# Optimization experiments

Hardware: AMD Instinct MI355X
Metric: run time of the kernel (lower is better)

The kernel has to match this reference:

```python
import jax, jax.numpy as jnp
import numpy as np

H = 128; F = 64; G = 50; L = 4; CUT = 10.0
M = 256; K = 8; A = 32
N_TOPO = M * A; N = M * K * A; NCONF = M * K
E_CONF = N * 16; E_GRAPH = N_TOPO * 4
ATOM_TYPES = 100; BOND_TYPES = 10
OFFSETS = jnp.linspace(0.0, CUT, G)
GCOEFF = -0.5 / (CUT / (G - 1)) ** 2  # GaussianSmearing coeff
BN_EPS = 1e-5


def batchnorm(x, g, b):
    # BatchNorm1d in training mode: batch statistics over nodes
    mu = x.mean(0)
    var = ((x - mu) ** 2).mean(0)
    return (x - mu) * jax.lax.rsqrt(var + BN_EPS) * g + b


def setup_inputs():
    key = jax.random.key(0)
    ks = jax.random.split(key, 20)
    s = lambda k, shp: (jax.random.normal(k, shp) * 0.05).astype(jnp.float32)
    inp = {}
    inp["x_topo"] = jax.random.randint(ks[0], (N_TOPO,), 0, ATOM_TYPES)
    inp["pos"] = jax.random.normal(ks[1], (N, 3), dtype=jnp.float32) * 3.0
    inp["edge_index_conf"] = jax.random.randint(ks[2], (2, E_CONF), 0, N)
    inp["edge_index_graph"] = jax.random.randint(ks[3], (2, E_GRAPH), 0, N_TOPO)
    inp["edge_attr_graph"] = jax.random.randint(ks[4], (E_GRAPH,), 0, BOND_TYPES)
    # conf_node_batch: for molecule i, repeat arange(A)+i*A over K conformers
    cnb = (np.arange(M)[:, None, None] * A + np.broadcast_to(np.arange(A), (K, A))).reshape(-1)
    inp["conf_node_batch"] = jnp.asarray(cnb, dtype=jnp.int32)
    inp["pos_batch"] = jnp.repeat(jnp.arange(NCONF), A).astype(jnp.int32)
    inp["conf_batch"] = jnp.repeat(jnp.arange(M), K).astype(jnp.int32)
    # parameters
    inp["atom_emb"] = s(ks[5], (ATOM_TYPES, H))
    inp["cf_lin1_w"] = s(ks[6], (L, H, F))
    inp["cf_mlp_w1"] = s(ks[7], (L, G, F)); inp["cf_mlp_b1"] = jnp.zeros((L, F), jnp.float32)
    inp["cf_mlp_w2"] = s(ks[8], (L, F, F)); inp["cf_mlp_b2"] = jnp.zeros((L, F), jnp.float32)
    inp["cf_lin2_w"] = s(ks[9], (L, F, H)); inp["cf_lin2_b"] = jnp.zeros((L, H), jnp.float32)
    inp["lin_w"] = s(ks[10], (L, H, H)); inp["lin_b"] = jnp.zeros((L, H), jnp.float32)
    inp["bond_emb"] = s(ks[11], (L, BOND_TYPES, H))
    inp["gin_w1"] = s(ks[12], (L, H, H)); inp["gin_b1"] = jnp.zeros((L, H), jnp.float32)
    inp["gin_w2"] = s(ks[13], (L, H, H)); inp["gin_b2"] = jnp.zeros((L, H), jnp.float32)
    inp["gin_bn_g"] = jnp.ones((L, H), jnp.float32); inp["gin_bn_b"] = jnp.zeros((L, H), jnp.float32)
    inp["bn_g"] = jnp.ones((L, H), jnp.float32); inp["bn_b"] = jnp.zeros((L, H), jnp.float32)
    inp["gin_eps"] = jnp.zeros((L,), jnp.float32)
    inp["out_w1"] = s(ks[14], (H, H)); inp["out_b1"] = jnp.zeros((H,), jnp.float32)
    inp["out_w2"] = s(ks[15], (H, 1)); inp["out_b2"] = jnp.zeros((1,), jnp.float32)
    return inp


def _forward(x_topo, edge_index_conf, edge_index_graph, edge_attr_graph,
             conf_node_batch, pos_batch, conf_batch,
             pos, atom_emb, cf_lin1_w, cf_mlp_w1, cf_mlp_b1, cf_mlp_w2, cf_mlp_b2,
             cf_lin2_w, cf_lin2_b, lin_w, lin_b, bond_emb,
             gin_w1, gin_b1, gin_w2, gin_b2, gin_bn_g, gin_bn_b, bn_g, bn_b,
             gin_eps, out_w1, out_b1, out_w2, out_b2):
    # AtomEncoder on topo graph, broadcast to all conformers
    x = atom_emb[x_topo][conf_node_batch]                      # [N, H]
    row, col = edge_index_conf[0], edge_index_conf[1]
    d = pos[row] - pos[col]
    ew = jnp.sqrt(jnp.sum(d * d, axis=-1) + 1e-12)             # edge_weight_conf [E_conf]
    ea = jnp.exp(GCOEFF * (ew[:, None] - OFFSETS) ** 2)        # GaussianSmearing [E_conf, G]
    cwin = 0.5 * (jnp.cos(ew * jnp.pi / CUT) + 1.0)            # SchNet cosine cutoff
    gr, gc = edge_index_graph[0], edge_index_graph[1]
    for l in range(L):
        # CFConv branch (use_conf)
        Wf = (jax.nn.relu(ea @ cf_mlp_w1[l] + cf_mlp_b1[l]) @ cf_mlp_w2[l] + cf_mlp_b2[l]) * cwin[:, None]
        h = x @ cf_lin1_w[l]                                   # lin1, no bias
        agg = jax.ops.segment_sum(h[row] * Wf, col, num_segments=N)
        h = agg @ cf_lin2_w[l] + cf_lin2_b[l]                  # lin2
        h = jax.nn.relu(h)
        h = h @ lin_w[l] + lin_b[l]
        out = x + h                                            # residual
        # GIN branch on topo graph (use_graph)
        x_agg = jax.ops.segment_max(x, conf_node_batch, num_segments=N_TOPO)
        eemb = bond_emb[l][edge_attr_graph]                    # BondEncoder
        magg = jax.ops.segment_sum(jax.nn.relu(x_agg[gr] + eemb), gc, num_segments=N_TOPO)
        hg = (1.0 + gin_eps[l]) * x_agg + magg
        hg = jax.nn.relu(batchnorm(hg @ gin_w1[l] + gin_b1[l], gin_bn_g[l], gin_bn_b[l]))
        hg = hg @ gin_w2[l] + gin_b2[l]
        hg = batchnorm(hg, bn_g[l], bn_b[l])
        out = out + hg[conf_node_batch]
        x = jax.nn.relu(out)
    x = jax.ops.segment_max(x, pos_batch, num_segments=NCONF)  # pool atoms -> conformers
    x = jax.ops.segment_max(x, conf_batch, num_segments=M)     # pool conformers -> molecules
    x = jax.nn.relu(x @ out_w1 + out_b1) @ out_w2 + out_b2     # out_layer
    return x                                                   # training mode: no clamp


def reference(x_topo, pos, edge_index_conf, edge_index_graph, edge_attr_graph,
              conf_node_batch, pos_batch, conf_batch,
              atom_emb, cf_lin1_w, cf_mlp_w1, cf_mlp_b1, cf_mlp_w2, cf_mlp_b2,
              cf_lin2_w, cf_lin2_b, lin_w, lin_b, bond_emb,
              gin_w1, gin_b1, gin_w2, gin_b2, gin_bn_g, gin_bn_b, bn_g, bn_b,
              gin_eps, out_w1, out_b1, out_w2, out_b2):
    return _forward(x_topo, edge_index_conf, edge_index_graph, edge_attr_graph,
                    conf_node_batch, pos_batch, conf_batch,
                    pos, atom_emb, cf_lin1_w, cf_mlp_w1, cf_mlp_b1, cf_mlp_w2, cf_mlp_b2,
                    cf_lin2_w, cf_lin2_b, lin_w, lin_b, bond_emb,
                    gin_w1, gin_b1, gin_w2, gin_b2, gin_bn_g, gin_bn_b, bn_g, bn_b,
                    gin_eps, out_w1, out_b1, out_w2, out_b2)
```

## Files before the change

kernel.cpp:

```cpp
#include <hip/hip_runtime.h>
#include <hip/hip_bf16.h>

#define EC 1048576
#define NN 65536
#define NT 8192
#define NCONF_ 2048
#define MM 256
#define HH 128
#define FF 64
#define GG 50
#define EG 32768

#define TBL 2048
#define TBL_SHIFT 11
#define TRANGE 14.0f

#define NEB (NN * 64 / 256)
#define SEB (8 * (EC / 256))

constexpr float STEP = 10.0f / 49.0f;
constexpr float GC = -0.5f / (STEP * STEP);

typedef __attribute__((ext_vector_type(8))) short bf16x8;
typedef __attribute__((ext_vector_type(4))) float f32x4;

__device__ __forceinline__ ushort f2b(float v) {
    __hip_bfloat16 h = __float2bfloat16(v);
    return *(ushort*)&h;
}
__device__ __forceinline__ float b2f(ushort u) {
    return __uint_as_float(((unsigned)u) << 16);
}

__global__ __launch_bounds__(256) void setup_kernel(
    const int* __restrict__ eic, const int* __restrict__ cnb,
    const int* __restrict__ eig, const float* __restrict__ pos,
    const float* __restrict__ emb, const int* __restrict__ xtopo,
    int* __restrict__ degA, int* __restrict__ degC,
    ushort* __restrict__ uu16, ushort* __restrict__ xb)
{
    int b = blockIdx.x, tid = threadIdx.x;
    if (b < EC / 256) {
        int e = b * 256 + tid;
        int r = eic[e], c = eic[EC + e];
        atomicAdd(&degA[c], 1);
        float dx = pos[r*3+0] - pos[c*3+0];
        float dy = pos[r*3+1] - pos[c*3+1];
        float dz = pos[r*3+2] - pos[c*3+2];
        float w = sqrtf(dx*dx + dy*dy + dz*dz + 1e-12f);
        float u = fminf(w * ((TBL - 1) / TRANGE), 2046.96875f);
        uu16[e] = (ushort)(int)(u * 32.0f);
    } else if (b < EC / 256 + EG / 256) {
        atomicAdd(&degC[eig[EG + (b - EC / 256) * 256 + tid]], 1);
    } else {
        int idx = (b - EC / 256 - EG / 256) * 256 + tid;
        int n = idx >> 7, f = idx & 127;
        xb[idx] = f2b(emb[xtopo[cnb[n]] * HH + f]);
    }
}

__device__ __forceinline__ void scan256(int* s, int tid) {
    for (int off = 1; off < 256; off <<= 1) {
        int t = (tid >= off) ? s[tid - off] : 0;
        __syncthreads();
        s[tid] += t;
        __syncthreads();
    }
}

__global__ __launch_bounds__(256) void scan1_all_kernel(
    const int* __restrict__ degA, const int* __restrict__ degC,
    int* __restrict__ offsA, int* __restrict__ offsC,
    int* __restrict__ bsumA, int* __restrict__ bsumC)
{
    __shared__ int s[256];
    int b = blockIdx.x, tid = threadIdx.x;
    const int* deg; int* offs; int* bsum;
    if (b < NN / 256) { deg = degA + b * 256; offs = offsA + b * 256; bsum = bsumA + b; }
    else { int bb = b - NN / 256; deg = degC + bb * 256; offs = offsC + bb * 256; bsum = bsumC + bb; }
    int v = deg[tid];
    s[tid] = v;
    __syncthreads();
    scan256(s, tid);
    offs[tid] = s[tid] - v;
    if (tid == 255) *bsum = s[255];
}

__global__ __launch_bounds__(256) void scan2_all_kernel(
    const int* __restrict__ bsumA, const int* __restrict__ bsumC,
    int* __restrict__ boffA, int* __restrict__ boffC)
{
    __shared__ int s[256];
    int b = blockIdx.x, tid = threadIdx.x;
    const int* bsum; int* boff; int nb;
    if (b == 0) { bsum = bsumA; boff = boffA; nb = NN / 256; }
    else        { bsum = bsumC; boff = boffC; nb = NT / 256; }
    int v = (tid < nb) ? bsum[tid] : 0;
    s[tid] = v;
    __syncthreads();
    scan256(s, tid);
    if (tid < nb) boff[tid] = s[tid] - v;
}

__global__ __launch_bounds__(256) void scan3_all_kernel(
    int* __restrict__ offsA, int* __restrict__ offsC,
    const int* __restrict__ boffA, const int* __restrict__ boffC,
    int* __restrict__ curA, int* __restrict__ curC)
{
    int b = blockIdx.x, tid = threadIdx.x;
    int* offs; const int* boff; int* cur; int i; int S, E;
    if (b < NN / 256) { i = b * 256 + tid; offs = offsA; boff = boffA; cur = curA; S = NN; E = EC; }
    else { i = (b - NN / 256) * 256 + tid; offs = offsC; boff = boffC; cur = curC; S = NT; E = EG; }
    int v = offs[i] + boff[i >> 8];
    offs[i] = v;
    cur[i] = v;
    if (i == 0) offs[S] = E;
}

__global__ __launch_bounds__(256) void scatter_all_kernel(
    const int* __restrict__ eic, const ushort* __restrict__ uu16,
    const int* __restrict__ eig, const int* __restrict__ eattr,
    int* __restrict__ curA, int* __restrict__ curC,
    int* __restrict__ pay_csr, int2* __restrict__ gpay)
{
    int b = blockIdx.x, tid = threadIdx.x;
    if (b < SEB) {
        int part = b & 7;
        int e = (b >> 3) * 256 + tid;
        int c = eic[EC + e];
        if ((c >> 13) != part) return;
        int p = atomicAdd(&curA[c], 1);
        pay_csr[p] = ((int)uu16[e] << 16) | (eic[e] & 0xFFFF);
    } else {
        int e = (b - SEB) * 256 + tid;
        int p = atomicAdd(&curC[eig[EG + e]], 1);
        gpay[p] = make_int2(eig[e], eattr[e]);
    }
}

__global__ __launch_bounds__(64) void build_table_kernel(
    const float* __restrict__ w1a, const float* __restrict__ b1a,
    const float* __restrict__ w2a, const float* __restrict__ b2a,
    float* __restrict__ table_all)
{
    int l = blockIdx.x >> TBL_SHIFT;
    int p = blockIdx.x & (TBL - 1);
    int lane = threadIdx.x;
    const float* w1 = w1a + (size_t)l * GG * FF;
    const float* b1 = b1a + (size_t)l * FF;
    const float* w2 = w2a + (size_t)l * FF * FF;
    const float* b2 = b2a + (size_t)l * FF;
    float w = p * (TRANGE / (TBL - 1));
    float t = b1[lane];
    for (int g = 0; g < GG; g++) {
        float d = w - g * STEP;
        float ea = __expf(GC * d * d);
        t = fmaf(ea, w1[g * 64 + lane], t);
    }
    __shared__ float ts[64];
    ts[lane] = fmaxf(t, 0.f);
    __syncthreads();
    float wf = b2[lane];
    for (int i = 0; i < 64; i++)
        wf = fmaf(ts[i], w2[i * 64 + lane], wf);
    float cw = 0.5f * (__cosf(w * (3.14159265358979323846f / 10.0f)) + 1.0f);
    table_all[((size_t)l * TBL + p) * 64 + lane] = wf * cw;
}

__global__ __launch_bounds__(256) void pack_table_kernel(
    const float* __restrict__ table_all, ushort2* __restrict__ table2_all)
{
    int idx = blockIdx.x * 256 + threadIdx.x;
    int f = idx & 63;
    int rest = idx >> 6;
    int i = rest & (TBL - 1);
    int l = rest >> TBL_SHIFT;
    const float* T = table_all + ((size_t)l * TBL) * 64;
    float t0 = T[(size_t)i * 64 + f];
    float t1 = (i + 1 < TBL) ? T[(size_t)(i + 1) * 64 + f] : 0.f;
    table2_all[idx] = make_ushort2(f2b(t0), f2b(t1 - t0));
}

__device__ __forceinline__ void prep_one(
    const float* __restrict__ W, ushort* __restrict__ Wf, int K, int N, int idx)
{
    int sz = K * N;
    int l = idx / sz;
    int t = idx - l * sz;
    int j = t & 7;
    int lane = (t >> 3) & 63;
    int rest = t >> 9;
    int KTl = K >> 5;
    int kt = rest % KTl;
    int nt = rest / KTl;
    int k = kt * 32 + (lane >> 4) * 8 + j;
    int n = nt * 16 + (lane & 15);
    Wf[idx] = f2b(W[(size_t)l * sz + (size_t)k * N + n]);
}

__global__ __launch_bounds__(256) void prep_all_kernel(
    const float* __restrict__ cf_lin1_w, const float* __restrict__ cf_lin2_w,
    const float* __restrict__ lin_w, const float* __restrict__ gin_w1,
    const float* __restrict__ gin_w2,
    ushort* __restrict__ w1f, ushort* __restrict__ w2f, ushort* __restrict__ wlf,
    ushort* __restrict__ gw1f, ushort* __restrict__ gw2f)
{
    int b = blockIdx.x, tid = threadIdx.x;
    if (b < 128)       prep_one(cf_lin1_w, w1f, HH, FF, b * 256 + tid);
    else if (b < 256)  prep_one(cf_lin2_w, w2f, FF, HH, (b - 128) * 256 + tid);
    else if (b < 512)  prep_one(lin_w, wlf, HH, HH, (b - 256) * 256 + tid);
    else if (b < 768)  prep_one(gin_w1, gw1f, HH, HH, (b - 512) * 256 + tid);
    else               prep_one(gin_w2, gw2f, HH, HH, (b - 768) * 256 + tid);
}

__global__ __launch_bounds__(256) void gemm_bf16_kernel(
    const ushort* __restrict__ A, const ushort* __restrict__ Bf,
    ushort* __restrict__ Cb)
{
    int tid = threadIdx.x;
    int wave = tid >> 6, lane = tid & 63;
    int m0 = (blockIdx.x * 4 + wave) * 16;
    int arow = m0 + (lane & 15);
    int ak = (lane >> 4) * 8;
    bf16x8 a[4];
    const ushort* Ap = A + (size_t)arow * 128 + ak;
    #pragma unroll
    for (int kt = 0; kt < 4; kt++)
        a[kt] = *(const bf16x8*)(Ap + kt * 32);
    f32x4 acc[4];
    #pragma unroll
    for (int i = 0; i < 4; i++) acc[i] = (f32x4){0.f, 0.f, 0.f, 0.f};
    const ushort* Bp = Bf + (size_t)lane * 8;
    #pragma unroll
    for (int nt = 0; nt < 4; nt++)
        #pragma unroll
        for (int kt = 0; kt < 4; kt++) {
            bf16x8 b = *(const bf16x8*)(Bp + ((size_t)(nt * 4 + kt)) * 512);
            acc[nt] = __builtin_amdgcn_mfma_f32_16x16x32_bf16(a[kt], b, acc[nt], 0, 0, 0);
        }
    int col0 = lane & 15;
    int rbase = m0 + (lane >> 4) * 4;
    #pragma unroll
    for (int nt = 0; nt < 4; nt++) {
        int col = nt * 16 + col0;
        #pragma unroll
        for (int r = 0; r < 4; r++)
            Cb[(size_t)(rbase + r) * 64 + col] = f2b(acc[nt][r]);
    }
}

__global__ __launch_bounds__(256) void edge_xagg_kernel(
    const int* __restrict__ offs, const int* __restrict__ pay_csr,
    const ushort2* __restrict__ table2, const ushort* __restrict__ h1b,
    ushort* __restrict__ aggb,
    const ushort* __restrict__ xb, ushort* __restrict__ xaggb)
{
    int tid = threadIdx.x;
    if (blockIdx.x < NEB) {
        int node = (blockIdx.x * 256 + tid) >> 6;
        int lane = tid & 63;
        int beg = offs[node], end = offs[node + 1];
        const float F32 = 0.03125f;
        float acc = 0.f;
        int p = beg;
        for (; p + 8 <= end; p += 8) {
            int pay[8];
            #pragma unroll
            for (int q = 0; q < 8; q++) pay[q] = pay_csr[p + q];
            float h[8];
            #pragma unroll
            for (int q = 0; q < 8; q++)
                h[q] = b2f(h1b[(size_t)(pay[q] & 0xFFFF) * 64 + lane]);
            int i0[8]; float fr[8];
            #pragma unroll
            for (int q = 0; q < 8; q++) {
                unsigned uf = (unsigned)pay[q] >> 16;
                i0[q] = uf >> 5;
                fr[q] = (float)(uf & 31) * F32;
            }
            ushort2 tt[8];
            #pragma unroll
            for (int q = 0; q < 8; q++)
                tt[q] = table2[(size_t)i0[q] * 64 + lane];
            #pragma unroll
            for (int q = 0; q < 8; q++)
                acc = fmaf(h[q], fmaf(b2f(tt[q].y), fr[q], b2f(tt[q].x)), acc);
        }
        for (; p < end; p++) {
            int pay = pay_csr[p];
            unsigned uf = (unsigned)pay >> 16;
            int i0 = uf >> 5;
            float fr = (float)(uf & 31) * F32;
            ushort2 tt = table2[(size_t)i0 * 64 + lane];
            acc = fmaf(b2f(h1b[(size_t)(pay & 0xFFFF) * 64 + lane]),
                       fmaf(b2f(tt.y), fr, b2f(tt.x)), acc);
        }
        aggb[(size_t)node * 64 + lane] = f2b(acc);
    } else {
        int idx = (blockIdx.x - NEB) * 256 + tid;
        int tn = idx >> 7, f = idx & 127;
        int m = tn >> 5, a = tn & 31;
        const ushort* base = xb + ((size_t)((m << 8) + a)) * HH + f;
        float mx = -3.4e38f;
        #pragma unroll
        for (int k = 0; k < 8; k++)
            mx = fmaxf(mx, b2f(base[(size_t)(k << 5) * HH]));
        xaggb[idx] = f2b(mx);
    }
}

#define TSTR 136

__global__ __launch_bounds__(256) void gin_gemm1_kernel(
    const int* __restrict__ goffs, const int2* __restrict__ gpay,
    const ushort* __restrict__ xaggb, const float* __restrict__ bemb,
    const float* __restrict__ eps, const ushort* __restrict__ Bf,
    const float* __restrict__ bias, ushort* __restrict__ Cb,
    float* __restrict__ gsum, float* __restrict__ gsq)
{
    __shared__ ushort hg0s[64 * TSTR];
    __shared__ float ssum[128], ssq[128];
    int tid = threadIdx.x;
    if (tid < 128) { ssum[tid] = 0.f; ssq[tid] = 0.f; }
    {
        int row = tid >> 2;
        int fc = (tid & 3) * 32;
        int tn = blockIdx.x * 64 + row;
        float e1 = 1.0f + eps[0];
        float acc[32];
        const ushort* xo = xaggb + (size_t)tn * HH + fc;
        #pragma unroll
        for (int c = 0; c < 4; c++) {
            bf16x8 x = *(const bf16x8*)(xo + c * 8);
            #pragma unroll
            for (int j = 0; j < 8; j++)
                acc[c * 8 + j] = e1 * b2f((ushort)x[j]);
        }
        int beg = goffs[tn], end = goffs[tn + 1];
        for (int p = beg; p < end; p++) {
            int2 g = gpay[p];
            const ushort* xs = xaggb + (size_t)g.x * HH + fc;
            const float* bs = bemb + (size_t)g.y * HH + fc;
            #pragma unroll
            for (int c = 0; c < 4; c++) {
                bf16x8 x = *(const bf16x8*)(xs + c * 8);
                float4 b0 = *(const float4*)(bs + c * 8);
                float4 b1 = *(const float4*)(bs + c * 8 + 4);
                float bb[8] = {b0.x, b0.y, b0.z, b0.w, b1.x, b1.y, b1.z, b1.w};
                #pragma unroll
                for (int j = 0; j < 8; j++)
                    acc[c * 8 + j] += fmaxf(b2f((ushort)x[j]) + bb[j], 0.f);
            }
        }
        ushort* dst = hg0s + row * TSTR + fc;
        #pragma unroll
        for (int j = 0; j < 32; j++) dst[j] = f2b(acc[j]);
    }
    __syncthreads();
    int wave = tid >> 6, lane = tid & 63;
    int lm = lane & 15, lq = lane >> 4;
    int ak = lq * 8;
    bf16x8 a[4];
    #pragma unroll
    for (int kt = 0; kt < 4; kt++)
        a[kt] = *(const bf16x8*)&hg0s[(wave * 16 + lm) * TSTR + ak + kt * 32];
    f32x4 acc[8];
    #pragma unroll
    for (int i = 0; i < 8; i++) acc[i] = (f32x4){0.f, 0.f, 0.f, 0.f};
    const ushort* Bp = Bf + (size_t)lane * 8;
    #pragma unroll
    for (int nt = 0; nt < 8; nt++)
        #pragma unroll
        for (int kt = 0; kt < 4; kt++) {
            bf16x8 b = *(const bf16x8*)(Bp + ((size_t)(nt * 4 + kt)) * 512);
            acc[nt] = __builtin_amdgcn_mfma_f32_16x16x32_bf16(a[kt], b, acc[nt], 0, 0, 0);
        }
    int rbase = blockIdx.x * 64 + wave * 16 + lq * 4;
    #pragma unroll
    for (int nt = 0; nt < 8; nt++) {
        int col = nt * 16 + lm;
        float bs = bias[col];
        float ps = 0.f, pq = 0.f;
        #pragma unroll
        for (int r = 0; r < 4; r++) {
            float v = acc[nt][r] + bs;
            Cb[(size_t)(rbase + r) * 128 + col] = f2b(v);
            ps += v; pq += v * v;
        }
        atomicAdd(&ssum[col], ps);
        atomicAdd(&ssq[col], pq);
    }
    __syncthreads();
    if (tid < 128) {
        atomicAdd(&gsum[tid], ssum[tid]);
        atomicAdd(&gsq[tid], ssq[tid]);
    }
}

__global__ __launch_bounds__(256) void gemm_bn_stats_kernel(
    const ushort* __restrict__ Araw, const float* __restrict__ sum1,
    const float* __restrict__ sq1, const float* __restrict__ g1,
    const float* __restrict__ bb1, const ushort* __restrict__ Bf,
    const float* __restrict__ bias, ushort* __restrict__ Cb,
    float* __restrict__ gsum, float* __restrict__ gsq)
{
    __shared__ float ssum[128], ssq[128];
    int tid = threadIdx.x;
    if (tid < 128) { ssum[tid] = 0.f; ssq[tid] = 0.f; }
    __syncthreads();
    int wave = tid >> 6, lane = tid & 63;
    int m0 = (blockIdx.x * 4 + wave) * 16;
    int arow = m0 + (lane & 15);
    int ak = (lane >> 4) * 8;
    const float INV_NT = 1.0f / NT;
    bf16x8 a[4];
    const ushort* Ap = Araw + (size_t)arow * 128 + ak;
    #pragma unroll
    for (int kt = 0; kt < 4; kt++) {
        bf16x8 raw = *(const bf16x8*)(Ap + kt * 32);
        ushort ub[8];
        #pragma unroll
        for (int j = 0; j < 8; j++) {
            int k = ak + kt * 32 + j;
            float mu = sum1[k] * INV_NT;
            float var = sq1[k] * INV_NT - mu * mu;
            float inv = rsqrtf(var + 1e-5f);
            float w = fmaxf((b2f((ushort)raw[j]) - mu) * inv * g1[k] + bb1[k], 0.f);
            ub[j] = f2b(w);
        }
        a[kt] = *(bf16x8*)ub;
    }
    f32x4 acc[8];
    #pragma unroll
    for (int i = 0; i < 8; i++) acc[i] = (f32x4){0.f, 0.f, 0.f, 0.f};
    const ushort* Bp = Bf + (size_t)lane * 8;
    #pragma unroll
    for (int nt = 0; nt < 8; nt++)
        #pragma unroll
        for (int kt = 0; kt < 4; kt++) {
            bf16x8 b = *(const bf16x8*)(Bp + ((size_t)(nt * 4 + kt)) * 512);
            acc[nt] = __builtin_amdgcn_mfma_f32_16x16x32_bf16(a[kt], b, acc[nt], 0, 0, 0);
        }
    int col0 = lane & 15;
    int rbase = m0 + (lane >> 4) * 4;
    #pragma unroll
    for (int nt = 0; nt < 8; nt++) {
        int col = nt * 16 + col0;
        float bs = bias[col];
        float ps = 0.f, pq = 0.f;
        #pragma unroll
        for (int r = 0; r < 4; r++) {
            float v = acc[nt][r] + bs;
            Cb[(size_t)(rbase + r) * 128 + col] = f2b(v);
            ps += v; pq += v * v;
        }
        atomicAdd(&ssum[col], ps);
        atomicAdd(&ssq[col], pq);
    }
    __syncthreads();
    if (tid < 128) {
        atomicAdd(&gsum[tid], ssum[tid]);
        atomicAdd(&gsq[tid], ssq[tid]);
    }
}

__global__ __launch_bounds__(256) void fused_lin_kernel(
    const ushort* __restrict__ aggb, const ushort* __restrict__ w2,
    const float* __restrict__ b2, const ushort* __restrict__ w3,
    const float* __restrict__ b3, const ushort* __restrict__ hgBb,
    const float* __restrict__ sum2, const float* __restrict__ sq2,
    const float* __restrict__ g2, const float* __restrict__ bb2,
    const int* __restrict__ cnb, const ushort* __restrict__ w1n,
    ushort* __restrict__ xb, ushort* __restrict__ h1b)
{
    __shared__ ushort t1s[4][16 * TSTR];
    __shared__ ushort t2s[4][16 * TSTR];
    int tid = threadIdx.x;
    int wave = tid >> 6, lane = tid & 63;
    int m0 = (blockIdx.x * 4 + wave) * 16;
    int lm = lane & 15;
    int lq = lane >> 4;
    ushort* T1 = t1s[wave];
    ushort* T2 = t2s[wave];
    const float INV_NT = 1.0f / NT;

    const ushort* Ap = aggb + (size_t)(m0 + lm) * 64 + lq * 8;
    bf16x8 a1[2];
    a1[0] = *(const bf16x8*)(Ap);
    a1[1] = *(const bf16x8*)(Ap + 32);
    f32x4 acc[8];
    #pragma unroll
    for (int i = 0; i < 8; i++) acc[i] = (f32x4){0.f, 0.f, 0.f, 0.f};
    {
        const ushort* Bp = w2 + (size_t)lane * 8;
        #pragma unroll
        for (int nt = 0; nt < 8; nt++)
            #pragma unroll
            for (int kt = 0; kt < 2; kt++) {
                bf16x8 b = *(const bf16x8*)(Bp + ((size_t)(nt * 2 + kt)) * 512);
                acc[nt] = __builtin_amdgcn_mfma_f32_16x16x32_bf16(a1[kt], b, acc[nt], 0, 0, 0);
            }
    }
    #pragma unroll
    for (int nt = 0; nt < 8; nt++) {
        int col = nt * 16 + lm;
        float bs = b2[col];
        #pragma unroll
        for (int r = 0; r < 4; r++) {
            float v = fmaxf(acc[nt][r] + bs, 0.f);
            T1[(lq * 4 + r) * TSTR + col] = f2b(v);
        }
    }
    __syncthreads();

    bf16x8 a2[4];
    #pragma unroll
    for (int kt = 0; kt < 4; kt++)
        a2[kt] = *(const bf16x8*)&T1[lm * TSTR + kt * 32 + lq * 8];
    __syncthreads();
    #pragma unroll
    for (int i = 0; i < 4; i++) {
        int idx = i * 64 + lane;
        int row = idx >> 4, ch = idx & 15;
        bf16x8 v = *(const bf16x8*)(xb + (size_t)(m0 + row) * HH + ch * 8);
        *(bf16x8*)&T1[row * TSTR + ch * 8] = v;
    }
    #pragma unroll
    for (int i = 0; i < 8; i++) acc[i] = (f32x4){0.f, 0.f, 0.f, 0.f};
    {
        const ushort* Bp = w3 + (size_t)lane * 8;
        #pragma unroll
        for (int nt = 0; nt < 8; nt++)
            #pragma unroll
            for (int kt = 0; kt < 4; kt++) {
                bf16x8 b = *(const bf16x8*)(Bp + ((size_t)(nt * 4 + kt)) * 512);
                acc[nt] = __builtin_amdgcn_mfma_f32_16x16x32_bf16(a2[kt], b, acc[nt], 0, 0, 0);
            }
    }
    int rbase = m0 + lq * 4;
    int cn[4];
    #pragma unroll
    for (int r = 0; r < 4; r++) cn[r] = cnb[rbase + r];
    #pragma unroll
    for (int nt = 0; nt < 8; nt++) {
        int col = nt * 16 + lm;
        float bs = b3[col];
        float mu2 = sum2[col] * INV_NT;
        float var2 = sq2[col] * INV_NT - mu2 * mu2;
        float sc2 = rsqrtf(var2 + 1e-5f) * g2[col];
        float sh2 = bb2[col] - mu2 * sc2;
        #pragma unroll
        for (int r = 0; r < 4; r++) {
            float v = acc[nt][r] + bs;
            v += b2f(T1[(lq * 4 + r) * TSTR + col]);
            v = fmaf(b2f(hgBb[(size_t)cn[r] * HH + col]), sc2, v + sh2);
            v = fmaxf(v, 0.f);
            T2[(lq * 4 + r) * TSTR + col] = f2b(v);
        }
    }
    __syncthreads();
    #pragma unroll
    for (int i = 0; i < 4; i++) {
        int idx = i * 64 + lane;
        int row = idx >> 4, ch = idx & 15;
        bf16x8 v = *(const bf16x8*)&T2[row * TSTR + ch * 8];
        *(bf16x8*)(xb + (size_t)(m0 + row) * HH + ch * 8) = v;
    }
    if (!w1n) return;
    __syncthreads();

    bf16x8 a3[4];
    #pragma unroll
    for (int kt = 0; kt < 4; kt++)
        a3[kt] = *(const bf16x8*)&T2[lm * TSTR + kt * 32 + lq * 8];
    f32x4 acc3[4];
    #pragma unroll
    for (int i = 0; i < 4; i++) acc3[i] = (f32x4){0.f, 0.f, 0.f, 0.f};
    {
        const ushort* Bp = w1n + (size_t)lane * 8;
        #pragma unroll
        for (int nt = 0; nt < 4; nt++)
            #pragma unroll
            for (int kt = 0; kt < 4; kt++) {
                bf16x8 b = *(const bf16x8*)(Bp + ((size_t)(nt * 4 + kt)) * 512);
                acc3[nt] = __builtin_amdgcn_mfma_f32_16x16x32_bf16(a3[kt], b, acc3[nt], 0, 0, 0);
            }
    }
    #pragma unroll
    for (int nt = 0; nt < 4; nt++) {
        int col = nt * 16 + lm;
        #pragma unroll
        for (int r = 0; r < 4; r++)
            T1[(lq * 4 + r) * TSTR + col] = f2b(acc3[nt][r]);
    }
    __syncthreads();
    #pragma unroll
    for (int i = 0; i < 2; i++) {
        int idx = i * 64 + lane;
        int row = idx >> 3, ch = idx & 7;
        bf16x8 v = *(const bf16x8*)&T1[row * TSTR + ch * 8];
        *(bf16x8*)(h1b + (size_t)(m0 + row) * FF + ch * 8) = v;
    }
}

__global__ __launch_bounds__(128) void out_layer_kernel(
    const ushort* __restrict__ xb, const float* __restrict__ w1,
    const float* __restrict__ b1, const float* __restrict__ w2,
    const float* __restrict__ b2, float* __restrict__ out)
{
    int m = blockIdx.x, f = threadIdx.x;
    const ushort* base = xb + (size_t)m * 256 * HH + f;
    float mx = -3.4e38f;
    for (int r = 0; r < 256; r++)
        mx = fmaxf(mx, b2f(base[(size_t)r * HH]));
    __shared__ float xs[128];
    xs[f] = mx;
    __syncthreads();
    float acc = b1[f];
    for (int k = 0; k < 128; k++) acc = fmaf(xs[k], w1[k * HH + f], acc);
    acc = fmaxf(acc, 0.f) * w2[f];
    __shared__ float red[128];
    red[f] = acc;
    __syncthreads();
    for (int off = 64; off > 0; off >>= 1) {
        if (f < off) red[f] += red[f + off];
        __syncthreads();
    }
    if (f == 0) out[m] = red[0] + b2[0];
}

extern "C" void kernel_launch(void* const* d_in, const int* in_sizes, int n_in,
                              void* d_out, int out_size, void* d_ws, size_t ws_size,
                              hipStream_t stream)
{
    const int*   x_topo    = (const int*)d_in[0];
    const float* pos       = (const float*)d_in[1];
    const int*   eic       = (const int*)d_in[2];
    const int*   eig       = (const int*)d_in[3];
    const int*   eattr     = (const int*)d_in[4];
    const int*   cnb       = (const int*)d_in[5];
    const float* atom_emb  = (const float*)d_in[8];
    const float* cf_lin1_w = (const float*)d_in[9];
    const float* cf_mlp_w1 = (const float*)d_in[10];
    const float* cf_mlp_b1 = (const float*)d_in[11];
    const float* cf_mlp_w2 = (const float*)d_in[12];
    const float* cf_mlp_b2 = (const float*)d_in[13];
    const float* cf_lin2_w = (const float*)d_in[14];
    const float* cf_lin2_b = (const float*)d_in[15];
    const float* lin_w     = (const float*)d_in[16];
    const float* lin_b     = (const float*)d_in[17];
    const float* bond_emb  = (const float*)d_in[18];
    const float* gin_w1    = (const float*)d_in[19];
    const float* gin_b1    = (const float*)d_in[20];
    const float* gin_w2    = (const float*)d_in[21];
    const float* gin_b2    = (const float*)d_in[22];
    const float* gin_bn_g  = (const float*)d_in[23];
    const float* gin_bn_b  = (const float*)d_in[24];
    const float* bn_g      = (const float*)d_in[25];
    const float* bn_b      = (const float*)d_in[26];
    const float* gin_eps   = (const float*)d_in[27];
    const float* out_w1    = (const float*)d_in[28];
    const float* out_b1    = (const float*)d_in[29];
    const float* out_w2    = (const float*)d_in[30];
    const float* out_b2    = (const float*)d_in[31];
    float* out = (float*)d_out;

    char* wsb = (char*)d_ws;
    size_t off = 0;
    auto alloc = [&](size_t nbytes) -> void* {
        void* p = (void*)(wsb + off);
        off += (nbytes + 255) & ~(size_t)255;
        return p;
    };
    ushort* uu16    = (ushort*)alloc(EC * 2);
    ushort* xb      = (ushort*)alloc((size_t)NN * HH * 2);
    ushort* h1b     = (ushort*)alloc((size_t)NN * FF * 2);
    ushort* aggb    = (ushort*)alloc((size_t)NN * FF * 2);
    ushort* xaggb   = (ushort*)alloc((size_t)NT * HH * 2);
    ushort* hgA     = (ushort*)alloc((size_t)NT * HH * 2);
    ushort* hgB     = (ushort*)alloc((size_t)NT * HH * 2);
    float*  table_all  = (float*)alloc((size_t)4 * TBL * 64 * 4);
    ushort2* table2_all = (ushort2*)alloc((size_t)4 * TBL * 64 * 4);
    float*  stats   = (float*)alloc((size_t)4 * 4 * 128 * 4);
    int*    degA    = (int*)alloc((size_t)(NN + NT) * 4);
    int*    degC    = degA + NN;
    int*    offsA   = (int*)alloc((NN + 1) * 4);
    int*    offsC   = (int*)alloc((NT + 1) * 4);
    int*    curA    = (int*)alloc(NN * 4);
    int*    curC    = (int*)alloc(NT * 4);
    int*    bsumA   = (int*)alloc(256 * 4);
    int*    bsumC   = (int*)alloc(256 * 4);
    int*    boffA   = (int*)alloc(256 * 4);
    int*    boffC   = (int*)alloc(256 * 4);
    int*    pay_csr = (int*)alloc((size_t)EC * 4);
    int2*   gpay    = (int2*)alloc((size_t)EG * 8);
    ushort* w1f     = (ushort*)alloc((size_t)4 * HH * FF * 2);
    ushort* w2f     = (ushort*)alloc((size_t)4 * FF * HH * 2);
    ushort* wlf     = (ushort*)alloc((size_t)4 * HH * HH * 2);
    ushort* gw1f    = (ushort*)alloc((size_t)4 * HH * HH * 2);
    ushort* gw2f    = (ushort*)alloc((size_t)4 * HH * HH * 2);

    hipMemsetAsync(stats, 0, (size_t)4 * 4 * 128 * 4 + (size_t)(NN + NT) * 4, stream);

    setup_kernel<<<EC / 256 + EG / 256 + NN * HH / 256, 256, 0, stream>>>(
        eic, cnb, eig, pos, atom_emb, x_topo, degA, degC, uu16, xb);
    scan1_all_kernel<<<NN / 256 + NT / 256, 256, 0, stream>>>(
        degA, degC, offsA, offsC, bsumA, bsumC);
    scan2_all_kernel<<<2, 256, 0, stream>>>(bsumA, bsumC, boffA, boffC);
    scan3_all_kernel<<<NN / 256 + NT / 256, 256, 0, stream>>>(
        offsA, offsC, boffA, boffC, curA, curC);
    scatter_all_kernel<<<SEB + EG / 256, 256, 0, stream>>>(
        eic, uu16, eig, eattr, curA, curC, pay_csr, gpay);

    build_table_kernel<<<4 * TBL, 64, 0, stream>>>(
        cf_mlp_w1, cf_mlp_b1, cf_mlp_w2, cf_mlp_b2, table_all);
    pack_table_kernel<<<4 * TBL * 64 / 256, 256, 0, stream>>>(table_all, table2_all);
    prep_all_kernel<<<1024, 256, 0, stream>>>(
        cf_lin1_w, cf_lin2_w, lin_w, gin_w1, gin_w2, w1f, w2f, wlf, gw1f, gw2f);

    gemm_bf16_kernel<<<NN / 64, 256, 0, stream>>>(xb, w1f, h1b);

    for (int l = 0; l < 4; l++) {
        const ushort2* table2 = table2_all + (size_t)l * TBL * 64;
        float* sum1 = stats + (size_t)l * 512;
        float* sq1  = sum1 + 128;
        float* sum2 = sum1 + 256;
        float* sq2  = sum1 + 384;
        edge_xagg_kernel<<<NEB + NT * HH / 256, 256, 0, stream>>>(
            offsA, pay_csr, table2, h1b, aggb, xb, xaggb);
        gin_gemm1_kernel<<<NT / 64, 256, 0, stream>>>(
            offsC, gpay, xaggb, bond_emb + (size_t)l * 10 * HH, gin_eps + l,
            gw1f + (size_t)l * HH * HH, gin_b1 + (size_t)l * HH, hgA, sum1, sq1);
        gemm_bn_stats_kernel<<<NT / 64, 256, 0, stream>>>(
            hgA, sum1, sq1, gin_bn_g + (size_t)l * HH, gin_bn_b + (size_t)l * HH,
            gw2f + (size_t)l * HH * HH, gin_b2 + (size_t)l * HH, hgB, sum2, sq2);
        fused_lin_kernel<<<NN / 64, 256, 0, stream>>>(
            aggb, w2f + (size_t)l * FF * HH, cf_lin2_b + (size_t)l * HH,
            wlf + (size_t)l * HH * HH, lin_b + (size_t)l * HH,
            hgB, sum2, sq2, bn_g + (size_t)l * HH, bn_b + (size_t)l * HH,
            cnb, (l < 3) ? (w1f + (size_t)(l + 1) * HH * FF) : nullptr,
            xb, h1b);
    }

    out_layer_kernel<<<MM, 128, 0, stream>>>(xb, out_w1, out_b1, out_w2, out_b2, out);
}
```

Baseline: 726.2 us.

## Replace conformer-edge CSR build with fixed-capacity padded slots plus overflow list

Conformer edges now go into per-node padded slots of capacity 32 through a single atomic counter per node. Edges beyond capacity go to a global overflow list, which high-degree nodes scan linearly in the aggregation kernel. This removes the degree-count atomics and the three-kernel multi-block prefix scan for the large edge set. The small graph-edge scan is collapsed into one single-block kernel. The trade-offs are a larger sparse payload buffer, a fixed-size overflow buffer with no bounds check, and a memset that assumes the allocator places buffers contiguously with 256-byte alignment.

Result: no change. 720.6 us (-0.8%).

```diff
diff --git a/kernel.cpp b/kernel.cpp
--- a/kernel.cpp
+++ b/kernel.cpp
@@ -4,7 +4,6 @@
 #define EC 1048576
 #define NN 65536
 #define NT 8192
-#define NCONF_ 2048
 #define MM 256
 #define HH 128
 #define FF 64
@@ -15,6 +14,7 @@
 #define TBL_SHIFT 11
 #define TRANGE 14.0f
 
+#define CAP 32
 #define NEB (NN * 64 / 256)
 #define SEB (8 * (EC / 256))
 
@@ -36,14 +36,12 @@
     const int* __restrict__ eic, const int* __restrict__ cnb,
     const int* __restrict__ eig, const float* __restrict__ pos,
     const float* __restrict__ emb, const int* __restrict__ xtopo,
-    int* __restrict__ degA, int* __restrict__ degC,
-    ushort* __restrict__ uu16, ushort* __restrict__ xb)
+    int* __restrict__ degC, ushort* __restrict__ uu16, ushort* __restrict__ xb)
 {
     int b = blockIdx.x, tid = threadIdx.x;
     if (b < EC / 256) {
         int e = b * 256 + tid;
         int r = eic[e], c = eic[EC + e];
-        atomicAdd(&degA[c], 1);
         float dx = pos[r*3+0] - pos[c*3+0];
         float dy = pos[r*3+1] - pos[c*3+1];
         float dz = pos[r*3+2] - pos[c*3+2];
@@ -59,69 +57,40 @@
     }
 }
 
-__device__ __forceinline__ void scan256(int* s, int tid) {
-    for (int off = 1; off < 256; off <<= 1) {
-        int t = (tid >= off) ? s[tid - off] : 0;
+__global__ __launch_bounds__(256) void scanC_kernel(
+    const int* __restrict__ degC, int* __restrict__ offsC, int* __restrict__ curC)
+{
+    __shared__ int s[256];
+    __shared__ int base;
+    int tid = threadIdx.x;
+    if (tid == 0) base = 0;
+    __syncthreads();
+    for (int c = 0; c < NT / 256; c++) {
+        int v = degC[c * 256 + tid];
+        s[tid] = v;
         __syncthreads();
-        s[tid] += t;
+        for (int off = 1; off < 256; off <<= 1) {
+            int t = (tid >= off) ? s[tid - off] : 0;
+            __syncthreads();
+            s[tid] += t;
+            __syncthreads();
+        }
+        int excl = s[tid] - v + base;
+        offsC[c * 256 + tid] = excl;
+        curC[c * 256 + tid] = excl;
         __syncthreads();
-    }
-}
-
-__global__ __launch_bounds__(256) void scan1_all_kernel(
-    const int* __restrict__ degA, const int* __restrict__ degC,
-    int* __restrict__ offsA, int* __restrict__ offsC,
-    int* __restrict__ bsumA, int* __restrict__ bsumC)
-{
-    __shared__ int s[256];
-    int b = blockIdx.x, tid = threadIdx.x;
-    const int* deg; int* offs; int* bsum;
-    if (b < NN / 256) { deg = degA + b * 256; offs = offsA + b * 256; bsum = bsumA + b; }
-    else { int bb = b - NN / 256; deg = degC + bb * 256; offs = offsC + bb * 256; bsum = bsumC + bb; }
-    int v = deg[tid];
-    s[tid] = v;
-    __syncthreads();
-    scan256(s, tid);
-    offs[tid] = s[tid] - v;
-    if (tid == 255) *bsum = s[255];
-}
-
-__global__ __launch_bounds__(256) void scan2_all_kernel(
-    const int* __restrict__ bsumA, const int* __restrict__ bsumC,
-    int* __restrict__ boffA, int* __restrict__ boffC)
-{
-    __shared__ int s[256];
-    int b = blockIdx.x, tid = threadIdx.x;
-    const int* bsum; int* boff; int nb;
-    if (b == 0) { bsum = bsumA; boff = boffA; nb = NN / 256; }
-    else        { bsum = bsumC; boff = boffC; nb = NT / 256; }
-    int v = (tid < nb) ? bsum[tid] : 0;
-    s[tid] = v;
-    __syncthreads();
-    scan256(s, tid);
-    if (tid < nb) boff[tid] = s[tid] - v;
-}
-
-__global__ __launch_bounds__(256) void scan3_all_kernel(
-    int* __restrict__ offsA, int* __restrict__ offsC,
-    const int* __restrict__ boffA, const int* __restrict__ boffC,
-    int* __restrict__ curA, int* __restrict__ curC)
-{
-    int b = blockIdx.x, tid = threadIdx.x;
-    int* offs; const int* boff; int* cur; int i; int S, E;
-    if (b < NN / 256) { i = b * 256 + tid; offs = offsA; boff = boffA; cur = curA; S = NN; E = EC; }
-    else { i = (b - NN / 256) * 256 + tid; offs = offsC; boff = boffC; cur = curC; S = NT; E = EG; }
-    int v = offs[i] + boff[i >> 8];
-    offs[i] = v;
-    cur[i] = v;
-    if (i == 0) offs[S] = E;
+        if (tid == 255) base += s[255];
+        __syncthreads();
+    }
+    if (tid == 0) offsC[NT] = EG;
 }
 
 __global__ __launch_bounds__(256) void scatter_all_kernel(
     const int* __restrict__ eic, const ushort* __restrict__ uu16,
     const int* __restrict__ eig, const int* __restrict__ eattr,
-    int* __restrict__ curA, int* __restrict__ curC,
-    int* __restrict__ pay_csr, int2* __restrict__ gpay)
+    int* __restrict__ cntA, int* __restrict__ curC,
+    int* __restrict__ pay_pad, int2* __restrict__ gpay,
+    int* __restrict__ ovf_cnt, int2* __restrict__ ovf)
 {
     int b = blockIdx.x, tid = threadIdx.x;
     if (b < SEB) {
@@ -129,8 +98,14 @@
         int e = (b >> 3) * 256 + tid;
         int c = eic[EC + e];
         if ((c >> 13) != part) return;
-        int p = atomicAdd(&curA[c], 1);
-        pay_csr[p] = ((int)uu16[e] << 16) | (eic[e] & 0xFFFF);
+        int pay = ((int)uu16[e] << 16) | (eic[e] & 0xFFFF);
+        int slot = atomicAdd(&cntA[c], 1);
+        if (slot < CAP) {
+            pay_pad[c * CAP + slot] = pay;
+        } else {
+            int o = atomicAdd(ovf_cnt, 1);
+            ovf[o] = make_int2(c, pay);
+        }
     } else {
         int e = (b - SEB) * 256 + tid;
         int p = atomicAdd(&curC[eig[EG + e]], 1);
@@ -250,7 +225,8 @@
 }
 
 __global__ __launch_bounds__(256) void edge_xagg_kernel(
-    const int* __restrict__ offs, const int* __restrict__ pay_csr,
+    const int* __restrict__ cntA, const int* __restrict__ pay_pad,
+    const int* __restrict__ ovf_cnt, const int2* __restrict__ ovf,
     const ushort2* __restrict__ table2, const ushort* __restrict__ h1b,
     ushort* __restrict__ aggb,
     const ushort* __restrict__ xb, ushort* __restrict__ xaggb)
@@ -259,14 +235,16 @@
     if (blockIdx.x < NEB) {
         int node = (blockIdx.x * 256 + tid) >> 6;
         int lane = tid & 63;
-        int beg = offs[node], end = offs[node + 1];
+        int deg = cntA[node];
+        int n1 = min(deg, CAP);
+        const int* pp = pay_pad + (size_t)node * CAP;
         const float F32 = 0.03125f;
         float acc = 0.f;
-        int p = beg;
-        for (; p + 8 <= end; p += 8) {
+        int p = 0;
+        for (; p + 8 <= n1; p += 8) {
             int pay[8];
             #pragma unroll
-            for (int q = 0; q < 8; q++) pay[q] = pay_csr[p + q];
+            for (int q = 0; q < 8; q++) pay[q] = pp[p + q];
             float h[8];
             #pragma unroll
             for (int q = 0; q < 8; q++)
@@ -286,14 +264,28 @@
             for (int q = 0; q < 8; q++)
                 acc = fmaf(h[q], fmaf(b2f(tt[q].y), fr[q], b2f(tt[q].x)), acc);
         }
-        for (; p < end; p++) {
-            int pay = pay_csr[p];
+        for (; p < n1; p++) {
+            int pay = pp[p];
             unsigned uf = (unsigned)pay >> 16;
             int i0 = uf >> 5;
             float fr = (float)(uf & 31) * F32;
             ushort2 tt = table2[(size_t)i0 * 64 + lane];
             acc = fmaf(b2f(h1b[(size_t)(pay & 0xFFFF) * 64 + lane]),
                        fmaf(b2f(tt.y), fr, b2f(tt.x)), acc);
+        }
+        if (deg > CAP) {
+            int no = *ovf_cnt;
+            for (int j = 0; j < no; j++) {
+                int2 o = ovf[j];
+                if (o.x == node) {
+                    unsigned uf = (unsigned)o.y >> 16;
+                    int i0 = uf >> 5;
+                    float fr = (float)(uf & 31) * F32;
+                    ushort2 tt = table2[(size_t)i0 * 64 + lane];
+                    acc = fmaf(b2f(h1b[(size_t)(o.y & 0xFFFF) * 64 + lane]),
+                               fmaf(b2f(tt.y), fr, b2f(tt.x)), acc);
+                }
+            }
         }
         aggb[(size_t)node * 64 + lane] = f2b(acc);
     } else {
@@ -682,17 +674,13 @@
     float*  table_all  = (float*)alloc((size_t)4 * TBL * 64 * 4);
     ushort2* table2_all = (ushort2*)alloc((size_t)4 * TBL * 64 * 4);
     float*  stats   = (float*)alloc((size_t)4 * 4 * 128 * 4);
-    int*    degA    = (int*)alloc((size_t)(NN + NT) * 4);
-    int*    degC    = degA + NN;
-    int*    offsA   = (int*)alloc((NN + 1) * 4);
+    int*    cntA    = (int*)alloc((size_t)NN * 4);
+    int*    degC    = (int*)alloc((size_t)NT * 4);
+    int*    ovf_cnt = (int*)alloc(256);
     int*    offsC   = (int*)alloc((NT + 1) * 4);
-    int*    curA    = (int*)alloc(NN * 4);
     int*    curC    = (int*)alloc(NT * 4);
-    int*    bsumA   = (int*)alloc(256 * 4);
-    int*    bsumC   = (int*)alloc(256 * 4);
-    int*    boffA   = (int*)alloc(256 * 4);
-    int*    boffC   = (int*)alloc(256 * 4);
-    int*    pay_csr = (int*)alloc((size_t)EC * 4);
+    int*    pay_pad = (int*)alloc((size_t)NN * CAP * 4);
+    int2*   ovf     = (int2*)alloc((size_t)8192 * 8);
     int2*   gpay    = (int2*)alloc((size_t)EG * 8);
     ushort* w1f     = (ushort*)alloc((size_t)4 * HH * FF * 2);
     ushort* w2f     = (ushort*)alloc((size_t)4 * FF * HH * 2);
@@ -700,17 +688,16 @@
     ushort* gw1f    = (ushort*)alloc((size_t)4 * HH * HH * 2);
     ushort* gw2f    = (ushort*)alloc((size_t)4 * HH * HH * 2);
 
-    hipMemsetAsync(stats, 0, (size_t)4 * 4 * 128 * 4 + (size_t)(NN + NT) * 4, stream);
+    hipMemsetAsync(stats, 0,
+        ((size_t)4 * 4 * 128 * 4 + 255 & ~(size_t)255) +
+        ((size_t)NN * 4 + 255 & ~(size_t)255) +
+        ((size_t)NT * 4 + 255 & ~(size_t)255) + 256, stream);
 
     setup_kernel<<<EC / 256 + EG / 256 + NN * HH / 256, 256, 0, stream>>>(
-        eic, cnb, eig, pos, atom_emb, x_topo, degA, degC, uu16, xb);
-    scan1_all_kernel<<<NN / 256 + NT / 256, 256, 0, stream>>>(
-        degA, degC, offsA, offsC, bsumA, bsumC);
-    scan2_all_kernel<<<2, 256, 0, stream>>>(bsumA, bsumC, boffA, boffC);
-    scan3_all_kernel<<<NN / 256 + NT / 256, 256, 0, stream>>>(
-        offsA, offsC, boffA, boffC, curA, curC);
+        eic, cnb, eig, pos, atom_emb, x_topo, degC, uu16, xb);
+    scanC_kernel<<<1, 256, 0, stream>>>(degC, offsC, curC);
     scatter_all_kernel<<<SEB + EG / 256, 256, 0, stream>>>(
-        eic, uu16, eig, eattr, curA, curC, pay_csr, gpay);
+        eic, uu16, eig, eattr, cntA, curC, pay_pad, gpay, ovf_cnt, ovf);
 
     build_table_kernel<<<4 * TBL, 64, 0, stream>>>(
         cf_mlp_w1, cf_mlp_b1, cf_mlp_w2, cf_mlp_b2, table_all);
@@ -727,7 +714,7 @@
         float* sum2 = sum1 + 256;
         float* sq2  = sum1 + 384;
         edge_xagg_kernel<<<NEB + NT * HH / 256, 256, 0, stream>>>(
-            offsA, pay_csr, table2, h1b, aggb, xb, xaggb);
+            cntA, pay_pad, ovf_cnt, ovf, table2, h1b, aggb, xb, xaggb);
         gin_gemm1_kernel<<<NT / 64, 256, 0, stream>>>(
             offsC, gpay, xaggb, bond_emb + (size_t)l * 10 * HH, gin_eps + l,
             gw1f + (size_t)l * HH * HH, gin_b1 + (size_t)l * HH, hgA, sum1, sq1);
```
